# Optimization experiments

Hardware: AMD Instinct MI355X
Metric: run time of the kernel (lower is better)

The kernel has to match this reference:

```python
import jax, jax.numpy as jnp
import numpy as np
from jax import lax

BIT_SIZE = 8
ES_SIZE = 1


def posit_quantize(x, nbits=BIT_SIZE, es=ES_SIZE):
    """Round x to the nearest posit(nbits, es) representable value (round-to-nearest
    of the fraction given the regime/exponent-dependent fraction width)."""
    sign = jnp.sign(x)
    a = jnp.abs(x)
    safe = jnp.where(a > 0, a, jnp.ones_like(a))
    logx = jnp.floor(jnp.log2(safe))            # binade exponent
    ipow = 2 ** es                               # 2^es, python int
    k = jnp.floor(logx / ipow)                   # regime value
    regime_len = jnp.where(k >= 0, k + 2, -k + 1)
    fbits = jnp.clip(nbits - 1 - regime_len - es, 0, 23)  # fraction bits left
    scale = jnp.exp2(logx)
    frac = safe / scale                          # in [1, 2)
    step = jnp.exp2(fbits)
    q = jnp.round(frac * step) / step * scale
    maxpos = jnp.float32(2.0 ** ((nbits - 2) * ipow))
    minpos = jnp.float32(2.0 ** (-(nbits - 2) * ipow))
    q = jnp.clip(q, minpos, maxpos)
    return jnp.where(a > 0, sign * q, jnp.zeros_like(x))


def pq(x):
    # straight-through quantizer (forward value is exact posit rounding)
    return x + lax.stop_gradient(posit_quantize(x) - x)


def conv2d(x, w):  # NCHW, OIHW, valid, stride 1
    return lax.conv_general_dilated(x, w, (1, 1), 'VALID',
                                    dimension_numbers=('NCHW', 'OIHW', 'NCHW'))


def maxpool2(x):
    return lax.reduce_window(x, -jnp.inf, lax.max,
                             (1, 1, 2, 2), (1, 1, 2, 2), 'VALID')


def setup_inputs() -> dict:
    key = jax.random.key(0)
    ks = jax.random.split(key, 9)
    B = 4096
    x = jax.random.normal(ks[0], (B, 1, 28, 28), jnp.float32)
    def init_w(k, shape, fan_in):
        bound = 1.0 / np.sqrt(fan_in)
        return jax.random.uniform(k, shape, jnp.float32, -bound, bound)
    conv1_w = init_w(ks[1], (32, 1, 3, 3), 1 * 9)
    conv1_b = init_w(ks[2], (32,), 1 * 9)
    conv2_w = init_w(ks[3], (64, 32, 3, 3), 32 * 9)
    conv2_b = init_w(ks[4], (64,), 32 * 9)
    fc1_w = init_w(ks[5], (128, 12 * 12 * 64), 12 * 12 * 64)
    fc1_b = init_w(ks[6], (128,), 12 * 12 * 64)
    fc2_w = init_w(ks[7], (10, 128), 128)
    fc2_b = init_w(ks[8], (10,), 128)
    return dict(x=x, conv1_w=conv1_w, conv1_b=conv1_b, conv2_w=conv2_w,
                conv2_b=conv2_b, fc1_w=fc1_w, fc1_b=fc1_b,
                fc2_w=fc2_w, fc2_b=fc2_b)


def reference(x, conv1_w, conv1_b, conv2_w, conv2_b, fc1_w, fc1_b, fc2_w, fc2_b):
    # PositizedConv2d: posit-quantize activations and weights, conv in fp32, add bias
    h = conv2d(pq(x), pq(conv1_w)) + conv1_b[None, :, None, None]   # [B,32,26,26]
    h = jax.nn.relu(h)
    h = conv2d(pq(h), pq(conv2_w)) + conv2_b[None, :, None, None]   # [B,64,24,24]
    h = jax.nn.relu(h)
    h = maxpool2(h)                                                  # [B,64,12,12]
    # dropout layers are identity in eval mode
    h = h.reshape(-1, 12 * 12 * 64)
    h = jax.nn.relu(jnp.dot(pq(h), pq(fc1_w).T) + fc1_b)             # [B,128]
    out = jnp.dot(pq(h), pq(fc2_w).T) + fc2_b                        # [B,10]
    return out
```

## Files before the change

### kernel.cpp

```cpp
#include <hip/hip_runtime.h>

using u16 = unsigned short;
using u32 = unsigned int;
typedef __attribute__((ext_vector_type(8))) short bf16x8;
typedef __attribute__((ext_vector_type(4))) float f32x4;

__device__ __forceinline__ float posit_q(float x) {
    float a = __builtin_fabsf(x);
    u32 u = __float_as_uint(a);
    int logx = (int)(u >> 23) - 127;
    logx = logx < -60 ? -60 : (logx > 60 ? 60 : logx);
    float frac = __uint_as_float((u & 0x007fffffu) | 0x3f800000u);
    int k = logx >> 1;
    int rl = (k >= 0) ? (k + 2) : (1 - k);
    int fb = 6 - rl; fb = fb < 0 ? 0 : fb;
    float step = (float)(1 << fb);
    float q = rintf(frac * step) * __uint_as_float((u32)(127 + logx - fb) << 23);
    q = fminf(fmaxf(q, 0x1p-12f), 0x1p12f);
    return (a > 0.0f) ? copysignf(q, x) : 0.0f;
}

__device__ __forceinline__ float b2f(u16 v) { return __uint_as_float((u32)v << 16); }
__device__ __forceinline__ u16 f2b(float f) { return (u16)(__float_as_uint(f) >> 16); }

__device__ __forceinline__ void lut_init(int tid, float* lut) {
    if (tid < 256) {
        int e = tid - 127;
        float m = 0.f;
        if (e >= -12 && e <= 12) {
            int k = e >> 1;
            int rl = max(k + 2, 1 - k);
            int fb = max(6 - rl, 0);
            m = __uint_as_float((u32)(150 + e - fb) << 23) * 1.5f;
        }
        lut[tid] = m;
    }
}
__device__ __forceinline__ u32 pq_pos_raw(float x, const float* __restrict__ lut) {
    u32 u = __float_as_uint(x);
    float c = lut[u >> 23];
    float q = (x + c) - c;
    q = fminf(fmaxf(q, 0x1p-12f), 0x1p12f);
    return u == 0u ? 0u : __float_as_uint(q);
}

__global__ __launch_bounds__(256) void prep_kernel(
    const float* __restrict__ w1, const float* __restrict__ w2,
    const float* __restrict__ fw2,
    float* __restrict__ w1q, u16* __restrict__ w2frag, float* __restrict__ fc2wq) {
    int i = blockIdx.x * 256 + threadIdx.x;
    if (i < 288)  w1q[i]   = posit_q(w1[i]);
    if (i < 1280) fc2wq[i] = posit_q(fw2[i]);
    if (i < 18432) {
        int e = i & 7, lane = (i >> 3) & 63, c9 = i >> 9;
        int kc = c9 % 9, nt = c9 / 9;
        int n = nt * 16 + (lane & 15);
        int ci = ((lane >> 4) << 3) + e;
        w2frag[i] = f2b(posit_q(w2[n * 288 + ci * 9 + kc]));
    }
}

__global__ __launch_bounds__(256) void prep2_kernel(
    const float* __restrict__ fw1, u16* __restrict__ fc1wqF) {
    int i = blockIdx.x * 256 + threadIdx.x;
    int e = i & 7, lane = (i >> 3) & 63, c = i >> 9;
    int kk = c % 288, nt = c / 288;
    int n = nt * 16 + (lane & 15);
    int k = kk * 32 + ((lane >> 4) << 3) + e;
    fc1wqF[i] = f2b(posit_q(fw1[(size_t)n * 9216 + k]));
}

#define PLS 5416
__global__ __launch_bounds__(512, 4) void conv_fused_kernel(
    const float* __restrict__ x, const float* __restrict__ w1q, const float* __restrict__ b1,
    const u16* __restrict__ w2frag, const float* __restrict__ b2,
    const float* __restrict__ fw1, u16* __restrict__ fc1wq, u16* __restrict__ pooled) {
    __shared__ __align__(16) float sX[784];
    __shared__ __align__(16) u16 sH1[4 * PLS];
    __shared__ __align__(16) u16 sPool[64 * 152];
    __shared__ float sLut[256];
    int img = blockIdx.x, tid = threadIdx.x;
    int wave = tid >> 6, lane = tid & 63;
    int col = lane & 15, quad = lane >> 4;

    lut_init(tid, sLut);

    for (int i = tid; i < 784; i += 512) sX[i] = posit_q(x[(size_t)img * 784 + i]);
    if (tid < 288) fc1wq[(size_t)img * 288 + tid] = f2b(posit_q(fw1[(size_t)img * 288 + tid]));

    int ocp = tid & 15;
    float wreg[18];
#pragma unroll
    for (int j = 0; j < 18; ++j) wreg[j] = w1q[ocp * 18 + j];
    float bias0 = b1[ocp * 2], bias1 = b1[ocp * 2 + 1];

    __syncthreads();

    int pgrp = tid >> 4;
    u16* h1dst = &sH1[(ocp >> 2) * PLS + 2 * (ocp & 3)];
    for (int it = 0; it < 22; ++it) {
        int p = it * 32 + pgrp;
        if (p < 676) {
            int y = p / 26, xx = p - y * 26;
            const float* px = &sX[y * 28 + xx];
            float in9[9];
#pragma unroll
            for (int r = 0; r < 3; ++r)
#pragma unroll
                for (int c = 0; c < 3; ++c) in9[r * 3 + c] = px[r * 28 + c];
            float a0 = bias0, a1 = bias1;
#pragma unroll
            for (int j = 0; j < 9; ++j) {
                a0 = fmaf(wreg[j], in9[j], a0);
                a1 = fmaf(wreg[9 + j], in9[j], a1);
            }
            u32 r0 = pq_pos_raw(fmaxf(a0, 0.f), sLut);
            u32 r1 = pq_pos_raw(fmaxf(a1, 0.f), sLut);
            *(u32*)&h1dst[p * 8] = (r0 >> 16) | (r1 & 0xFFFF0000u);
        }
    }

    __syncthreads();
    int npair = wave & 1, mq = wave >> 1;
    bf16x8 bfrag[2][9];
#pragma unroll
    for (int j = 0; j < 2; ++j)
#pragma unroll
        for (int kc = 0; kc < 9; ++kc)
            bfrag[j][kc] = *(const bf16x8*)(w2frag + (((npair * 2 + j) * 9 + kc) * 64 + lane) * 8);
    float cb0 = b2[(npair * 2) * 16 + col];
    float cb1 = b2[(npair * 2 + 1) * 16 + col];
    int poolb0 = ((npair * 2) * 16 + col) * 152;
    int poolb1 = ((npair * 2 + 1) * 16 + col) * 152;
    const u16* aplane = &sH1[quad * PLS];

    for (int t = 0; t < 9; ++t) {
        int mt = mq * 9 + t;
        int m = mt * 16 + col;
        int pp = m >> 2, wi = m & 3;
        int py = pp / 12, px_ = pp - py * 12;
        int oh = 2 * py + (wi >> 1), ow = 2 * px_ + (wi & 1);
        const u16* ap = aplane + (oh * 26 + ow) * 8;
        f32x4 acc0 = {0.f, 0.f, 0.f, 0.f}, acc1 = {0.f, 0.f, 0.f, 0.f};
#pragma unroll
        for (int kc = 0; kc < 9; ++kc) {
            int kh = kc / 3, kw = kc - kh * 3;
            bf16x8 af = *(const bf16x8*)(ap + (kh * 26 + kw) * 8);
            acc0 = __builtin_amdgcn_mfma_f32_16x16x32_bf16(af, bfrag[0][kc], acc0, 0, 0, 0);
            acc1 = __builtin_amdgcn_mfma_f32_16x16x32_bf16(af, bfrag[1][kc], acc1, 0, 0, 0);
        }
        float mx0 = fmaxf(fmaxf(acc0[0], acc0[1]), fmaxf(acc0[2], acc0[3]));
        float mx1 = fmaxf(fmaxf(acc1[0], acc1[1]), fmaxf(acc1[2], acc1[3]));
        sPool[poolb0 + mt * 4 + quad] = (u16)(pq_pos_raw(fmaxf(mx0 + cb0, 0.f), sLut) >> 16);
        sPool[poolb1 + mt * 4 + quad] = (u16)(pq_pos_raw(fmaxf(mx1 + cb1, 0.f), sLut) >> 16);
    }
    __syncthreads();

    for (int u = tid; u < 1152; u += 512) {
        int c = u / 18, g = u - c * 18;
        uint4 v = *(const uint4*)&sPool[c * 152 + g * 8];
        *(uint4*)(pooled + (size_t)img * 9216 + c * 144 + g * 8) = v;
    }
}

#define AS 2328
__global__ __launch_bounds__(512, 4) void fc1_part_kernel(const u16* __restrict__ pooled,
    const u16* __restrict__ fc1wqF, float* __restrict__ part) {
    __shared__ __align__(16) char smem[16 * AS * 2];
    u16* sA = (u16*)smem;
    float* sAcc = (float*)smem;
    int blk = blockIdx.x, tid = threadIdx.x;
    int mb = blk >> 2, ks = blk & 3;
    int wave = tid >> 6, lane = tid & 63;
    int row = lane & 15, quad = lane >> 4;

    {
        const u16* src = pooled + (size_t)mb * 16 * 9216 + ks * 2304;
        for (int i = tid; i < 4608; i += 512) {
            int r = i / 288, o = i - r * 288;
            *(uint4*)&sA[r * AS + o * 8] = *(const uint4*)(src + (size_t)r * 9216 + o * 8);
        }
    }
    __syncthreads();

    const bf16x8* bbase = (const bf16x8*)fc1wqF + (size_t)(ks * 72 + wave * 9) * 64 + lane;
    const u16* abase = &sA[row * AS + wave * 288 + quad * 8];
    f32x4 acc[8];
#pragma unroll
    for (int nt = 0; nt < 8; ++nt) acc[nt] = f32x4{0.f, 0.f, 0.f, 0.f};
#pragma unroll 1
    for (int k2 = 0; k2 < 9; ++k2) {
        bf16x8 a = *(const bf16x8*)(abase + k2 * 32);
        bf16x8 b[8];
#pragma unroll
        for (int nt = 0; nt < 8; ++nt)
            b[nt] = bbase[((size_t)nt * 288 + k2) * 64];
#pragma unroll
        for (int nt = 0; nt < 8; ++nt)
            acc[nt] = __builtin_amdgcn_mfma_f32_16x16x32_bf16(a, b[nt], acc[nt], 0, 0, 0);
    }
    __syncthreads();
    if (wave < 4) {
#pragma unroll
        for (int nt = 0; nt < 8; ++nt)
#pragma unroll
            for (int r = 0; r < 4; ++r)
                sAcc[wave * 2112 + (quad * 4 + r) * 132 + nt * 16 + row] = acc[nt][r];
    }
    __syncthreads();
    if (wave >= 4) {
#pragma unroll
        for (int nt = 0; nt < 8; ++nt)
#pragma unroll
            for (int r = 0; r < 4; ++r)
                sAcc[(wave - 4) * 2112 + (quad * 4 + r) * 132 + nt * 16 + row] += acc[nt][r];
    }
    __syncthreads();
    for (int e = tid; e < 2048; e += 512) {
        int o = (e >> 7) * 132 + (e & 127);
        part[(size_t)blk * 2048 + e] = sAcc[o] + sAcc[2112 + o] + sAcc[4224 + o] + sAcc[6336 + o];
    }
}

__global__ __launch_bounds__(256) void fc2_red_kernel(const float* __restrict__ part,
    const float* __restrict__ fc1b, const float* __restrict__ fc2wq,
    const float* __restrict__ fc2b, float* __restrict__ out) {
    __shared__ __align__(16) u16 sFc1[2048];
    __shared__ float sW2[1280];
    __shared__ float sB2[16];
    __shared__ float sLut[256];
    int mb = blockIdx.x, tid = threadIdx.x;
    lut_init(tid, sLut);
    for (int i = tid; i < 1280; i += 256) sW2[i] = fc2wq[i];
    if (tid < 10) sB2[tid] = fc2b[tid];
    __syncthreads();
    const float* pb = part + (size_t)mb * 4 * 2048;
    for (int e = tid; e < 2048; e += 256) {
        float s = pb[e] + pb[2048 + e] + pb[4096 + e] + pb[6144 + e];
        sFc1[e] = (u16)(pq_pos_raw(fmaxf(s + fc1b[e & 127], 0.f), sLut) >> 16);
    }
    __syncthreads();
    if (tid < 160) {
        int il = tid / 10, oc = tid - il * 10;
        float s = sB2[oc];
        const u16* hp = &sFc1[il * 128];
        const float* wp = &sW2[oc * 128];
#pragma unroll
        for (int k = 0; k < 128; ++k) s = fmaf(b2f(hp[k]), wp[k], s);
        out[(size_t)(mb * 16 + il) * 10 + oc] = s;
    }
}

extern "C" void kernel_launch(void* const* d_in, const int* in_sizes, int n_in,
                              void* d_out, int out_size, void* d_ws, size_t ws_size,
                              hipStream_t stream) {
    const float* x    = (const float*)d_in[0];
    const float* w1   = (const float*)d_in[1];
    const float* b1   = (const float*)d_in[2];
    const float* w2   = (const float*)d_in[3];
    const float* b2   = (const float*)d_in[4];
    const float* fw1  = (const float*)d_in[5];
    const float* fb1  = (const float*)d_in[6];
    const float* fw2  = (const float*)d_in[7];
    const float* fb2  = (const float*)d_in[8];
    float* out = (float*)d_out;

    char* ws = (char*)d_ws;
    float* w1q     = (float*)(ws + 0);
    float* fc2wq   = (float*)(ws + 1280);
    u16*   w2frag  = (u16*)(ws + 6400);
    u16*   fc1wqF  = (u16*)(ws + 43520);
    u16*   fc1dmy  = (u16*)(ws + 2402816);
    u16*   pooled  = (u16*)(ws + 4762112);
    float* part    = (float*)(ws + 80259584);

    prep_kernel<<<72, 256, 0, stream>>>(w1, w2, fw2, w1q, w2frag, fc2wq);
    prep2_kernel<<<4608, 256, 0, stream>>>(fw1, fc1wqF);
    conv_fused_kernel<<<4096, 512, 0, stream>>>(x, w1q, b1, w2frag, b2, fw1, fc1dmy, pooled);
    fc1_part_kernel<<<1024, 512, 0, stream>>>(pooled, fc1wqF, part);
    fc2_red_kernel<<<256, 256, 0, stream>>>(part, fb1, fc2wq, fb2, out);
}
```

Baseline: 250.7 us.

## Re-tile conv2 MFMA loop so each wave computes 4 M-tiles by all 64 channels

Instead of each wave owning 2 of the 4 output-channel tiles and looping over 9 M-tiles, each of the 8 waves now computes 4 M-tiles across all 4 channel tiles in a 4x4 register-blocked accumulator. The 36 M-tiles are covered as 32 in the main block plus 4 handled by the first four waves. Each A fragment read from shared memory is reused across 4 channel tiles, halving LDS reads, and B fragments are loaded per kc from global/cache instead of being held in registers. This raises accumulator register pressure (64 floats) and leaves some waves with a tail imbalance.

```diff
diff --git a/kernel.cpp b/kernel.cpp
--- a/kernel.cpp
+++ b/kernel.cpp
@@ -121,38 +121,82 @@
     }
 
     __syncthreads();
-    int npair = wave & 1, mq = wave >> 1;
-    bf16x8 bfrag[2][9];
-#pragma unroll
-    for (int j = 0; j < 2; ++j)
-#pragma unroll
-        for (int kc = 0; kc < 9; ++kc)
-            bfrag[j][kc] = *(const bf16x8*)(w2frag + (((npair * 2 + j) * 9 + kc) * 64 + lane) * 8);
-    float cb0 = b2[(npair * 2) * 16 + col];
-    float cb1 = b2[(npair * 2 + 1) * 16 + col];
-    int poolb0 = ((npair * 2) * 16 + col) * 152;
-    int poolb1 = ((npair * 2 + 1) * 16 + col) * 152;
+
+    int mq = wave;
+    float cb[4];
+    int poolb[4];
+#pragma unroll
+    for (int j = 0; j < 4; ++j) {
+        cb[j] = b2[j * 16 + col];
+        poolb[j] = (j * 16 + col) * 152;
+    }
     const u16* aplane = &sH1[quad * PLS];
 
-    for (int t = 0; t < 9; ++t) {
-        int mt = mq * 9 + t;
+    {
+        f32x4 acc[4][4];
+#pragma unroll
+        for (int t = 0; t < 4; ++t)
+#pragma unroll
+            for (int j = 0; j < 4; ++j) acc[t][j] = f32x4{0.f, 0.f, 0.f, 0.f};
+        int aoff[4];
+#pragma unroll
+        for (int t = 0; t < 4; ++t) {
+            int m = (mq * 4 + t) * 16 + col;
+            int pp = m >> 2, wi = m & 3;
+            int py = pp / 12, px_ = pp - py * 12;
+            int oh = 2 * py + (wi >> 1), ow = 2 * px_ + (wi & 1);
+            aoff[t] = (oh * 26 + ow) * 8;
+        }
+#pragma unroll
+        for (int kc = 0; kc < 9; ++kc) {
+            int kh = kc / 3, kw = kc - kh * 3;
+            bf16x8 bf[4];
+#pragma unroll
+            for (int j = 0; j < 4; ++j)
+                bf[j] = *(const bf16x8*)(w2frag + (((j * 9 + kc) * 64) + lane) * 8);
+#pragma unroll
+            for (int t = 0; t < 4; ++t) {
+                bf16x8 af = *(const bf16x8*)(aplane + aoff[t] + (kh * 26 + kw) * 8);
+#pragma unroll
+                for (int j = 0; j < 4; ++j)
+                    acc[t][j] = __builtin_amdgcn_mfma_f32_16x16x32_bf16(af, bf[j], acc[t][j], 0, 0, 0);
+            }
+        }
+#pragma unroll
+        for (int t = 0; t < 4; ++t) {
+            int mt = mq * 4 + t;
+#pragma unroll
+            for (int j = 0; j < 4; ++j) {
+                float mx = fmaxf(fmaxf(acc[t][j][0], acc[t][j][1]), fmaxf(acc[t][j][2], acc[t][j][3]));
+                sPool[poolb[j] + mt * 4 + quad] = (u16)(pq_pos_raw(fmaxf(mx + cb[j], 0.f), sLut) >> 16);
+            }
+        }
+    }
+    if (wave < 4) {
+        int mt = 32 + wave;
+        f32x4 acc[4];
+#pragma unroll
+        for (int j = 0; j < 4; ++j) acc[j] = f32x4{0.f, 0.f, 0.f, 0.f};
         int m = mt * 16 + col;
         int pp = m >> 2, wi = m & 3;
         int py = pp / 12, px_ = pp - py * 12;
         int oh = 2 * py + (wi >> 1), ow = 2 * px_ + (wi & 1);
-        const u16* ap = aplane + (oh * 26 + ow) * 8;
-        f32x4 acc0 = {0.f, 0.f, 0.f, 0.f}, acc1 = {0.f, 0.f, 0.f, 0.f};
+        int aoff = (oh * 26 + ow) * 8;
 #pragma unroll
         for (int kc = 0; kc < 9; ++kc) {
             int kh = kc / 3, kw = kc - kh * 3;
-            bf16x8 af = *(const bf16x8*)(ap + (kh * 26 + kw) * 8);
-            acc0 = __builtin_amdgcn_mfma_f32_16x16x32_bf16(af, bfrag[0][kc], acc0, 0, 0, 0);
-            acc1 = __builtin_amdgcn_mfma_f32_16x16x32_bf16(af, bfrag[1][kc], acc1, 0, 0, 0);
-        }
-        float mx0 = fmaxf(fmaxf(acc0[0], acc0[1]), fmaxf(acc0[2], acc0[3]));
-        float mx1 = fmaxf(fmaxf(acc1[0], acc1[1]), fmaxf(acc1[2], acc1[3]));
-        sPool[poolb0 + mt * 4 + quad] = (u16)(pq_pos_raw(fmaxf(mx0 + cb0, 0.f), sLut) >> 16);
-        sPool[poolb1 + mt * 4 + quad] = (u16)(pq_pos_raw(fmaxf(mx1 + cb1, 0.f), sLut) >> 16);
+            bf16x8 af = *(const bf16x8*)(aplane + aoff + (kh * 26 + kw) * 8);
+#pragma unroll
+            for (int j = 0; j < 4; ++j) {
+                bf16x8 bf = *(const bf16x8*)(w2frag + (((j * 9 + kc) * 64) + lane) * 8);
+                acc[j] = __builtin_amdgcn_mfma_f32_16x16x32_bf16(af, bf, acc[j], 0, 0, 0);
+            }
+        }
+#pragma unroll
+        for (int j = 0; j < 4; ++j) {
+            float mx = fmaxf(fmaxf(acc[j][0], acc[j][1]), fmaxf(acc[j][2], acc[j][3]));
+            sPool[poolb[j] + mt * 4 + quad] = (u16)(pq_pos_raw(fmaxf(mx + cb[j], 0.f), sLut) >> 16);
+        }
     }
     __syncthreads();
 
```

New measurement: 261.7 us. 1.04x slower.
